# Kernel optimization log

Measured on AMD Instinct MI355X. Metric: run time of the kernel, lower is better.

Reference implementation:

```python
import jax, jax.numpy as jnp
import numpy as np

B, N, T, E, EH, C = 32, 500, 13, 2000, 300, 40
EPS = 1e-5


def _bn_noaffine(x):
    m = x.mean(axis=(0, 2, 3), keepdims=True)
    v = x.var(axis=(0, 2, 3), keepdims=True)
    return (x - m) * jax.lax.rsqrt(v + EPS)


def _bn(x, g, b):
    return g[None, :, None, None] * _bn_noaffine(x) + b[None, :, None, None]


def _conv1x1(x, W, b):
    # x: [B,Cin,N,T], W: [Cout,Cin]
    return jnp.einsum('bcnt,oc->bont', x, W) + b[None, :, None, None]


def _dconv(x, W, b, dil=2):
    # dilated causal conv, kernel (1,2): W [Cout,Cin,2]
    y = jnp.einsum('bcnt,oc->bont', x[..., :-dil], W[:, :, 0])
    y = y + jnp.einsum('bcnt,oc->bont', x[..., dil:], W[:, :, 1])
    return y + b[None, :, None, None]


def setup_inputs() -> dict:
    key = jax.random.key(0)
    ks = jax.random.split(key, 24)
    d = {}
    d['input'] = jax.random.normal(ks[0], (B, 1, N, T), jnp.float32)
    d['A_fwd'] = jax.random.uniform(ks[1], (N, N), jnp.float32) / N
    d['A_bwd'] = jax.random.uniform(ks[2], (N, N), jnp.float32) / N
    d['indices'] = jax.random.randint(ks[3], (2, E), 0, N, jnp.int32)
    d['G0_all'] = jax.random.uniform(ks[4], (E, EH), jnp.float32) * 0.01
    d['G1_all'] = jax.random.uniform(ks[5], (EH, E), jnp.float32) * 0.01
    d['nodevec1'] = jax.random.normal(ks[6], (N, 10), jnp.float32)
    d['nodevec2'] = jax.random.normal(ks[7], (10, N), jnp.float32)
    d['w_edge_f'] = jax.random.uniform(ks[8], (EH,), jnp.float32)
    d['w_edge_b'] = jax.random.uniform(ks[9], (EH,), jnp.float32)
    d['vsrc_f'] = jax.random.normal(ks[10], (3, C), jnp.float32) * 0.05
    d['vdst_f'] = jax.random.normal(ks[11], (3, C), jnp.float32) * 0.05
    d['vsrc_b'] = jax.random.normal(ks[12], (3, C), jnp.float32) * 0.05
    d['vdst_b'] = jax.random.normal(ks[13], (3, C), jnp.float32) * 0.05
    d['start_w'] = jax.random.normal(ks[14], (C, 1), jnp.float32)
    d['start_b'] = jnp.zeros((C,), jnp.float32)
    d['filter_w'] = jax.random.normal(ks[15], (3, C, C, 2), jnp.float32) * (1.0 / np.sqrt(2 * C))
    d['filter_b'] = jnp.zeros((3, C), jnp.float32)
    d['gate_w'] = jax.random.normal(ks[16], (3, C, C, 2), jnp.float32) * (1.0 / np.sqrt(2 * C))
    d['gate_b'] = jnp.zeros((3, C), jnp.float32)
    d['gconv_w'] = jax.random.normal(ks[17], (3, 7 * C, C), jnp.float32) * (1.0 / np.sqrt(7 * C))
    d['gconv_b'] = jnp.zeros((3, C), jnp.float32)
    d['bn_g_gamma'] = jnp.ones((3, C), jnp.float32)
    d['bn_g_beta'] = jnp.zeros((3, C), jnp.float32)
    d['bn_gamma'] = jnp.ones((3, C), jnp.float32)
    d['bn_beta'] = jnp.zeros((3, C), jnp.float32)
    d['skip_w'] = jax.random.normal(ks[18], (3, 320, C), jnp.float32) * (1.0 / np.sqrt(C))
    d['skip_b'] = jnp.zeros((3, 320), jnp.float32)
    d['end1_w'] = jax.random.normal(ks[19], (640, 320), jnp.float32) * (1.0 / np.sqrt(320))
    d['end1_b'] = jnp.zeros((640,), jnp.float32)
    d['end2_w'] = jax.random.normal(ks[20], (12, 640), jnp.float32) * (1.0 / np.sqrt(640))
    d['end2_b'] = jnp.zeros((12,), jnp.float32)
    return d


def reference(input, A_fwd, A_bwd, indices, G0_all, G1_all, nodevec1, nodevec2,
              w_edge_f, w_edge_b, vsrc_f, vdst_f, vsrc_b, vdst_b,
              start_w, start_b, filter_w, filter_b, gate_w, gate_b,
              gconv_w, gconv_b, bn_g_gamma, bn_g_beta, bn_gamma, bn_beta,
              skip_w, skip_b, end1_w, end1_b, end2_w, end2_b):
    x = _bn_noaffine(input)
    x = _conv1x1(x, start_w, start_b)
    b, _, n, _ = x.shape
    # adaptive adjacency: softmax(relu(V1 @ V2)) over rows (torch dim=1 on [N,N])
    adp = jax.nn.softmax(jax.nn.relu(nodevec1 @ nodevec2), axis=1)
    # hypergraph edge-to-edge diffusion operators: G0 @ diag(w) @ G1  ->  [E,E]
    GG_f = G0_all @ (w_edge_f[:, None] * G1_all)
    GG_b = G0_all @ (w_edge_b[:, None] * G1_all)
    i0, i1 = indices[0], indices[1]
    eye = jnp.eye(n, dtype=x.dtype)
    skip = None
    for blk in range(3):
        # dynamic edge scores from node features (mean over time)
        xmean = x.mean(axis=3)                              # [B,C,N]
        src = xmean[:, :, i0]                               # [B,C,E]
        dst = xmean[:, :, i1]
        sc_f = jnp.einsum('bce,c->be', src, vsrc_f[blk]) + jnp.einsum('bce,c->be', dst, vdst_f[blk])
        sc_b = jnp.einsum('bce,c->be', src, vsrc_b[blk]) + jnp.einsum('bce,c->be', dst, vdst_b[blk])
        ef = jax.nn.sigmoid(sc_f @ GG_f)                    # [B,E]
        eb = jax.nn.sigmoid(sc_b @ GG_b)
        # identity medium with sigmoid edge weights scattered at the edge indices
        Mf = jnp.broadcast_to(eye, (b, n, n)).at[:, i0, i1].set(ef)
        Mb = jnp.broadcast_to(eye, (b, n, n)).at[:, i0, i1].set(eb)
        s0 = Mf * A_fwd[None]                               # [B,N,N]
        s1 = jnp.swapaxes(Mb, 1, 2) * A_bwd[None]
        s2 = jnp.broadcast_to(adp, (b, n, n))
        residual = x
        f = jnp.tanh(_dconv(residual, filter_w[blk], filter_b[blk]))
        g = jax.nn.sigmoid(_dconv(residual, gate_w[blk], gate_b[blk]))
        x = f * g
        # diffusion graph conv, order 2, over 3 batched supports
        outs = [x]
        for A in (s0, s1, s2):
            x1 = jnp.einsum('bcnt,bnm->bcmt', x, A)
            outs.append(x1)
            outs.append(jnp.einsum('bcnt,bnm->bcmt', x1, A))
        h = jnp.concatenate(outs, axis=1)                   # [B,7C,N,T']
        x = jnp.einsum('bcnt,co->bont', h, gconv_w[blk]) + gconv_b[blk][None, :, None, None]
        x = _bn(x, bn_g_gamma[blk], bn_g_beta[blk])
        x = x + residual[:, :, :, -x.shape[3]:]
        x = _bn(x, bn_gamma[blk], bn_beta[blk])
        s = _conv1x1(x, skip_w[blk], skip_b[blk])
        skip = s if skip is None else s + skip[:, :, :, -s.shape[3]:]
    x = jax.nn.leaky_relu(skip)
    x = jax.nn.leaky_relu(_conv1x1(x, end1_w, end1_b))
    x = _conv1x1(x, end2_w, end2_b)
    return x
```

## Files before the change

### kernel.cpp

```cpp
#include <hip/hip_runtime.h>
#include <hip/hip_bf16.h>

constexpr int B_  = 32;
constexpr int N_  = 500;
constexpr int T0_ = 13;
constexpr int E_  = 2000;
constexpr int EH_ = 300;
constexpr int C_  = 40;
constexpr float EPS_ = 1e-5f;
constexpr int KP_ = 512;

typedef short bf16x8 __attribute__((ext_vector_type(8)));
typedef _Float16 f16x8 __attribute__((ext_vector_type(8)));
typedef float f32x4  __attribute__((ext_vector_type(4)));

__device__ __forceinline__ float sigm(float x){ return 1.f/(1.f+__expf(-x)); }
__device__ __forceinline__ float lrelu(float x){ return x > 0.f ? x : 0.01f*x; }
__device__ __forceinline__ unsigned short f2bf(float f){
    __hip_bfloat16 h = __float2bfloat16(f);
    return *(unsigned short*)&h;
}
__device__ __forceinline__ float bf2f(unsigned short us){
    __hip_bfloat16 h = *(__hip_bfloat16*)&us;
    return __bfloat162float(h);
}

__global__ __launch_bounds__(256) void kern_init(float* __restrict__ insum, int* __restrict__ map,
                                                 int* __restrict__ cnts, int* __restrict__ selfe,
                                                 int* __restrict__ adpTbz)
{
    int i = blockIdx.x*256 + threadIdx.x;
    if (i < 2) insum[i] = 0.f;
    if (i < N_*N_) map[i] = -1;
    if (i < 1024) cnts[i] = 0;
    if (i < 512) selfe[i] = -1;
    if (i < KP_*KP_/2) adpTbz[i] = 0;
}

__global__ __launch_bounds__(256) void kern_zeroacc(float* __restrict__ p, int n)
{
    int i = blockIdx.x*256 + threadIdx.x;
    if (i < n) p[i] = 0.f;
}

__global__ __launch_bounds__(256) void kern_instats(const float* __restrict__ in, float* __restrict__ acc)
{
    float s = 0.f, ss = 0.f;
    int total = B_*N_*T0_;
    for (int i = blockIdx.x*256 + threadIdx.x; i < total; i += gridDim.x*256) {
        float v = in[i]; s += v; ss += v*v;
    }
    __shared__ float l1[256], l2[256];
    l1[threadIdx.x] = s; l2[threadIdx.x] = ss; __syncthreads();
    for (int o = 128; o > 0; o >>= 1) {
        if (threadIdx.x < o) { l1[threadIdx.x] += l1[threadIdx.x+o]; l2[threadIdx.x] += l2[threadIdx.x+o]; }
        __syncthreads();
    }
    if (threadIdx.x == 0) { atomicAdd(&acc[0], l1[0]); atomicAdd(&acc[1], l2[0]); }
}

__global__ __launch_bounds__(256) void kern_x0(const float* __restrict__ in, const float* __restrict__ insum,
    const float* __restrict__ sw, const float* __restrict__ sb, float* __restrict__ x)
{
    int idx = blockIdx.x*256 + threadIdx.x;
    int total = B_*N_*T0_*C_;
    if (idx >= total) return;
    float cnt = (float)(B_*N_*T0_);
    float mean = insum[0]/cnt;
    float var  = insum[1]/cnt - mean*mean;
    float inv  = rsqrtf(var + EPS_);
    int c = idx % C_;
    int pos = idx / C_;
    float xn = (in[pos] - mean)*inv;
    x[idx] = sw[c]*xn + sb[c];
}

__global__ __launch_bounds__(512) void kern_adp(const float* __restrict__ nv1, const float* __restrict__ nv2,
                                                __hip_bfloat16* __restrict__ adpTb)
{
    int n = blockIdx.x;
    int m = threadIdx.x;
    float r = 0.f;
    if (m < N_) {
        #pragma unroll
        for (int k = 0; k < 10; ++k) r += nv1[n*10+k]*nv2[k*N_+m];
        r = r > 0.f ? r : 0.f;
    }
    __shared__ float red[512];
    red[threadIdx.x] = (m < N_) ? r : -1e30f; __syncthreads();
    for (int o = 256; o > 0; o >>= 1) {
        if (threadIdx.x < o) red[threadIdx.x] = fmaxf(red[threadIdx.x], red[threadIdx.x+o]);
        __syncthreads();
    }
    float mx = red[0]; __syncthreads();
    float ev = (m < N_) ? __expf(r - mx) : 0.f;
    red[threadIdx.x] = ev; __syncthreads();
    for (int o = 256; o > 0; o >>= 1) {
        if (threadIdx.x < o) red[threadIdx.x] += red[threadIdx.x+o];
        __syncthreads();
    }
    float sum = red[0];
    if (m < N_) adpTb[(size_t)m*KP_ + n] = __float2bfloat16(ev/sum);
}

__global__ void kern_emax(const int* __restrict__ idx, int* __restrict__ map)
{
    int e = blockIdx.x*256 + threadIdx.x;
    if (e < E_) atomicMax(&map[idx[e]*N_ + idx[E_+e]], e);
}
__global__ void kern_ecnt(const int* __restrict__ idx, const int* __restrict__ map,
                          int* __restrict__ cnt0, int* __restrict__ cnt1, int* __restrict__ selfe)
{
    int e = blockIdx.x*256 + threadIdx.x;
    if (e >= E_) return;
    int i0 = idx[e], i1 = idx[E_+e];
    if (map[i0*N_+i1] != e) return;
    atomicAdd(&cnt1[i1], 1);
    atomicAdd(&cnt0[i0], 1);
    if (i0 == i1) selfe[i0] = e;
}
__global__ __launch_bounds__(512) void kern_scan(const int* __restrict__ cnt0, const int* __restrict__ cnt1,
    int* __restrict__ ptr0, int* __restrict__ ptr1, int* __restrict__ cur0, int* __restrict__ cur1)
{
    __shared__ int s0[512], s1[512];
    int tid = threadIdx.x;
    s0[tid] = (tid < N_) ? cnt0[tid] : 0;
    s1[tid] = (tid < N_) ? cnt1[tid] : 0;
    __syncthreads();
    for (int o = 1; o < 512; o <<= 1) {
        int v0 = (tid >= o) ? s0[tid-o] : 0;
        int v1 = (tid >= o) ? s1[tid-o] : 0;
        __syncthreads();
        s0[tid] += v0; s1[tid] += v1;
        __syncthreads();
    }
    if (tid == 0) { ptr0[0] = 0; ptr1[0] = 0; }
    if (tid < N_) {
        ptr0[tid+1] = s0[tid]; ptr1[tid+1] = s1[tid];
        cur0[tid] = (tid == 0) ? 0 : s0[tid-1];
        cur1[tid] = (tid == 0) ? 0 : s1[tid-1];
    }
}
__global__ void kern_efill(const int* __restrict__ idx, const int* __restrict__ map,
    const float* __restrict__ Af, const float* __restrict__ Ab,
    int* __restrict__ cur0, int* __restrict__ cur1,
    int* __restrict__ e0id, int* __restrict__ e0nb, float* __restrict__ a0v,
    int* __restrict__ e1id, int* __restrict__ e1nb, float* __restrict__ a1v)
{
    int e = blockIdx.x*256 + threadIdx.x;
    if (e >= E_) return;
    int i0 = idx[e], i1 = idx[E_+e];
    if (map[i0*N_+i1] != e) return;
    int s1 = atomicAdd(&cur1[i1], 1);
    e0id[s1] = e; e0nb[s1] = i0; a0v[s1] = Af[i0*N_+i1];
    int s0 = atomicAdd(&cur0[i0], 1);
    e1id[s0] = e; e1nb[s0] = i1; a1v[s0] = Ab[i1*N_+i0];
}

__global__ __launch_bounds__(64) void kern_umean(const float* __restrict__ x, int Tin,
    const float* __restrict__ vsf, const float* __restrict__ vdf,
    const float* __restrict__ vsb, const float* __restrict__ vdb,
    float* __restrict__ usf, float* __restrict__ udf, float* __restrict__ usb, float* __restrict__ udb)
{
    int bn = blockIdx.x;
    const float* xp = x + (size_t)bn*Tin*C_;
    int tid = threadIdx.x;
    float a0=0.f,a1=0.f,a2=0.f,a3=0.f;
    for (int i = tid; i < Tin*C_; i += 64) {
        float v = xp[i]; int c = i % C_;
        a0 += v*vsf[c]; a1 += v*vdf[c]; a2 += v*vsb[c]; a3 += v*vdb[c];
    }
    for (int o = 32; o > 0; o >>= 1) {
        a0 += __shfl_down(a0,o); a1 += __shfl_down(a1,o);
        a2 += __shfl_down(a2,o); a3 += __shfl_down(a3,o);
    }
    if (tid == 0) {
        float inv = 1.f/(float)Tin;
        usf[bn]=a0*inv; udf[bn]=a1*inv; usb[bn]=a2*inv; udb[bn]=a3*inv;
    }
}

__global__ void kern_sc(const int* __restrict__ idx,
    const float* __restrict__ usf, const float* __restrict__ udf,
    const float* __restrict__ usb, const float* __restrict__ udb,
    float* __restrict__ scf, float* __restrict__ scb)
{
    int i = blockIdx.x*256 + threadIdx.x;
    if (i >= B_*E_) return;
    int b = i / E_, e = i % E_;
    int i0 = idx[e], i1 = idx[E_+e];
    scf[i] = usf[b*N_+i0] + udf[b*N_+i1];
    scb[i] = usb[b*N_+i0] + udb[b*N_+i1];
}

__global__ __launch_bounds__(320) void kern_t(const float* __restrict__ scf, const float* __restrict__ scb,
    const float* __restrict__ G0, float* __restrict__ tf, float* __restrict__ tb)
{
    int b = blockIdx.x, chunk = blockIdx.y;
    int e0 = chunk*250;
    __shared__ float sf[250], sb2[250];
    int tid = threadIdx.x;
    for (int i = tid; i < 250; i += 320) { sf[i] = scf[b*E_+e0+i]; sb2[i] = scb[b*E_+e0+i]; }
    __syncthreads();
    if (tid < EH_) {
        float af = 0.f, ab = 0.f;
        for (int i = 0; i < 250; ++i) {
            float g = G0[(size_t)(e0+i)*EH_ + tid];
            af += sf[i]*g; ab += sb2[i]*g;
        }
        atomicAdd(&tf[b*EH_+tid], af);
        atomicAdd(&tb[b*EH_+tid], ab);
    }
}

__global__ __launch_bounds__(256) void kern_ef(const float* __restrict__ tf, const float* __restrict__ tb,
    const float* __restrict__ wf, const float* __restrict__ wb, const float* __restrict__ G1,
    float* __restrict__ ef, float* __restrict__ eb)
{
    int b = blockIdx.y;
    int e = blockIdx.x*256 + threadIdx.x;
    __shared__ float f[EH_], g[EH_];
    for (int i = threadIdx.x; i < EH_; i += 256) {
        f[i] = tf[b*EH_+i]*wf[i];
        g[i] = tb[b*EH_+i]*wb[i];
    }
    __syncthreads();
    if (e < E_) {
        float af = 0.f, ab = 0.f;
        for (int h = 0; h < EH_; ++h) {
            float v = G1[(size_t)h*E_ + e];
            af += f[h]*v; ab += g[h]*v;
        }
        ef[b*E_+e] = sigm(af);
        eb[b*E_+e] = sigm(ab);
    }
}

__global__ __launch_bounds__(256) void kern_dconv_acc(const float* __restrict__ x, int Tin,
    const float* __restrict__ fw, const float* __restrict__ fb4,
    const float* __restrict__ gw, const float* __restrict__ gb4,
    const float* __restrict__ wl0, const float* __restrict__ gbias,
    float* __restrict__ xg, float* __restrict__ gc,
    __hip_bfloat16* __restrict__ xgT, int JP)
{
    int Tout = Tin - 2;
    int nout = Tout*C_;
    int tile = threadIdx.x >> 7;
    int lane = threadIdx.x & 127;
    int bn = blockIdx.x*2 + tile;
    int b = bn / N_, n = bn % N_;
    __shared__ alignas(16) float xs[2][T0_*C_];
    __shared__ alignas(16) float wf[2*C_*C_];
    __shared__ alignas(16) float wg[2*C_*C_];
    __shared__ alignas(16) float wl[C_*C_];
    __shared__ alignas(16) float ps[2][11*C_];
    int tid = threadIdx.x;
    {
        const float4* xp = (const float4*)(x + (size_t)bn*Tin*C_);
        float4* xd = (float4*)xs[tile];
        for (int i = lane; i < (Tin*C_)/4; i += 128) xd[i] = xp[i];
    }
    for (int i = tid; i < 2*C_*C_; i += 256) {
        int k = i / (C_*C_); int r = i % (C_*C_); int c = r / C_; int o = r % C_;
        wf[i] = fw[(o*C_+c)*2 + k];
        wg[i] = gw[(o*C_+c)*2 + k];
    }
    for (int i = tid; i < C_*C_; i += 256) wl[i] = wl0[i];
    __syncthreads();
    int nq = Tout*10;
    for (int u = lane; u < nq; u += 128) {
        int t = u/10, o = (u%10)*4;
        float4 f4 = *(const float4*)&fb4[o];
        float4 g4 = *(const float4*)&gb4[o];
        for (int c = 0; c < C_; ++c) {
            float x0v = xs[tile][t*C_+c], x2v = xs[tile][(t+2)*C_+c];
            float4 wf0 = *(const float4*)&wf[c*C_+o];
            float4 wf1 = *(const float4*)&wf[C_*C_ + c*C_+o];
            float4 wg0 = *(const float4*)&wg[c*C_+o];
            float4 wg1 = *(const float4*)&wg[C_*C_ + c*C_+o];
            f4.x += wf0.x*x0v + wf1.x*x2v;  f4.y += wf0.y*x0v + wf1.y*x2v;
            f4.z += wf0.z*x0v + wf1.z*x2v;  f4.w += wf0.w*x0v + wf1.w*x2v;
            g4.x += wg0.x*x0v + wg1.x*x2v;  g4.y += wg0.y*x0v + wg1.y*x2v;
            g4.z += wg0.z*x0v + wg1.z*x2v;  g4.w += wg0.w*x0v + wg1.w*x2v;
        }
        float4 r4;
        r4.x = tanhf(f4.x)*sigm(g4.x);
        r4.y = tanhf(f4.y)*sigm(g4.y);
        r4.z = tanhf(f4.z)*sigm(g4.z);
        r4.w = tanhf(f4.w)*sigm(g4.w);
        *(float4*)&ps[tile][t*C_+o] = r4;
        *(float4*)&xg[(size_t)bn*nout + t*C_+o] = r4;
        int j = t*C_+o;
        size_t tb = ((size_t)b*JP + j)*KP_ + n;
        xgT[tb]          = __float2bfloat16(r4.x);
        xgT[tb + KP_]    = __float2bfloat16(r4.y);
        xgT[tb + 2*KP_]  = __float2bfloat16(r4.z);
        xgT[tb + 3*KP_]  = __float2bfloat16(r4.w);
    }
    __syncthreads();
    for (int u = lane; u < nq; u += 128) {
        int t = u/10, o = (u%10)*4;
        float4 a4 = *(const float4*)&gbias[o];
        for (int c = 0; c < C_; ++c) {
            float s = ps[tile][t*C_+c];
            float4 w = *(const float4*)&wl[c*C_+o];
            a4.x += s*w.x; a4.y += s*w.y; a4.z += s*w.z; a4.w += s*w.w;
        }
        *(float4*)&gc[(size_t)bn*nout + t*C_+o] = a4;
    }
}

__global__ __launch_bounds__(256) void kern_sparse_acc(const float* __restrict__ in,
    float* __restrict__ outTile, int Tout,
    const int* __restrict__ ptr, const int* __restrict__ nbr, const int* __restrict__ eid,
    const float* __restrict__ aval, const float* __restrict__ coef,
    const float* __restrict__ Amat, const int* __restrict__ selfe,
    const float* __restrict__ gwp, float* __restrict__ gc)
{
    int tile = threadIdx.x >> 7;
    int lane = threadIdx.x & 127;
    int bn = blockIdx.x*2 + tile;
    int b = bn / N_, m = bn % N_;
    __shared__ float wv[2][64];
    __shared__ int   nb[2][64];
    __shared__ alignas(16) float ps[2][11*C_];
    __shared__ alignas(16) float wl[C_*C_];
    int tid = threadIdx.x;
    int p0 = ptr[m], p1 = ptr[m+1];
    int deg = p1 - p0; if (deg > 64) deg = 64;
    if (lane < deg) {
        wv[tile][lane] = coef[b*E_ + eid[p0+lane]] * aval[p0+lane];
        nb[tile][lane] = nbr[p0+lane];
    }
    for (int i = tid; i < C_*C_; i += 256) wl[i] = gwp[i];
    __syncthreads();
    float dval = (selfe[m] >= 0) ? 0.f : Amat[(size_t)m*N_ + m];
    const float* inb = in + (size_t)b*N_*Tout*C_;
    int nout = Tout*C_;
    for (int oi = lane; oi < nout; oi += 128) {
        float acc = dval * inb[(size_t)m*nout + oi];
        for (int j = 0; j < deg; ++j) acc += wv[tile][j]*inb[(size_t)nb[tile][j]*nout + oi];
        ps[tile][oi] = acc;
        if (outTile) outTile[(size_t)bn*nout + oi] = acc;
    }
    __syncthreads();
    int nq = Tout*10;
    for (int u = lane; u < nq; u += 128) {
        int t = u/10, o = (u%10)*4;
        float4 a4 = *(const float4*)&gc[(size_t)bn*nout + t*C_+o];
        for (int c = 0; c < C_; ++c) {
            float s = ps[tile][t*C_+c];
            float4 w = *(const float4*)&wl[c*C_+o];
            a4.x += s*w.x; a4.y += s*w.y; a4.z += s*w.z; a4.w += s*w.w;
        }
        *(float4*)&gc[(size_t)bn*nout + t*C_+o] = a4;
    }
}

__global__ __launch_bounds__(256) void kern_gemm_mfma(const __hip_bfloat16* __restrict__ adpTb,
    const __hip_bfloat16* __restrict__ inT, float* __restrict__ outF,
    __hip_bfloat16* __restrict__ outT, int LD, int JP)
{
    int tid = threadIdx.x;
    int wave = tid >> 6, lane = tid & 63;
    int rn = lane & 15, q = lane >> 4;
    int b = blockIdx.z;
    int m0 = blockIdx.x*64;
    int j0 = blockIdx.y*64;
    const short* Ap = (const short*)adpTb + (size_t)(m0 + wave*16 + rn)*KP_ + q*8;
    bf16x8 areg[16];
    #pragma unroll
    for (int kk = 0; kk < 16; ++kk) areg[kk] = *(const bf16x8*)(Ap + kk*32);
    const short* Bp = (const short*)inT + ((size_t)b*JP + j0 + rn)*KP_ + q*8;
    f32x4 acc[4] = {};
    #pragma unroll
    for (int kk = 0; kk < 16; ++kk) {
        #pragma unroll
        for (int s = 0; s < 4; ++s) {
            bf16x8 bb = *(const bf16x8*)(Bp + (size_t)s*16*KP_ + kk*32);
            acc[s] = __builtin_amdgcn_mfma_f32_16x16x32_bf16(areg[kk], bb, acc[s], 0, 0, 0);
        }
    }
    int mb = m0 + wave*16 + q*4;
    #pragma unroll
    for (int s = 0; s < 4; ++s) {
        int j = j0 + s*16 + rn;
        if (j >= LD) continue;
        #pragma unroll
        for (int r = 0; r < 4; ++r) {
            int m = mb + r;
            if (m < N_) outF[((size_t)b*N_ + m)*LD + j] = acc[s][r];
        }
        if (outT) {
            ushort4 v;
            v.x = f2bf(acc[s][0]); v.y = f2bf(acc[s][1]);
            v.z = f2bf(acc[s][2]); v.w = f2bf(acc[s][3]);
            *(ushort4*)((unsigned short*)outT + ((size_t)b*JP + j)*KP_ + mb) = v;
        }
    }
}

__global__ __launch_bounds__(256) void kern_gacc(const float* __restrict__ part, const float* __restrict__ gwp,
    float* __restrict__ gc, int Tout)
{
    int tile = threadIdx.x >> 7;
    int lane = threadIdx.x & 127;
    int bn = blockIdx.x*2 + tile;
    int nout = Tout*C_;
    __shared__ alignas(16) float ps[2][11*C_];
    __shared__ alignas(16) float wl[C_*C_];
    int tid = threadIdx.x;
    {
        const float4* pp = (const float4*)(part + (size_t)bn*nout);
        float4* pd = (float4*)ps[tile];
        for (int i = lane; i < nout/4; i += 128) pd[i] = pp[i];
    }
    for (int i = tid; i < C_*C_; i += 256) wl[i] = gwp[i];
    __syncthreads();
    int nq = Tout*10;
    for (int u = lane; u < nq; u += 128) {
        int t = u/10, o = (u%10)*4;
        float4 a4 = *(const float4*)&gc[(size_t)bn*nout + t*C_+o];
        for (int c = 0; c < C_; ++c) {
            float s = ps[tile][t*C_+c];
            float4 w = *(const float4*)&wl[c*C_+o];
            a4.x += s*w.x; a4.y += s*w.y; a4.z += s*w.z; a4.w += s*w.w;
        }
        *(float4*)&gc[(size_t)bn*nout + t*C_+o] = a4;
    }
}

__global__ __launch_bounds__(320) void kern_bnstats(const float* __restrict__ src, size_t total, float* __restrict__ acc)
{
    int tid = threadIdx.x;
    float s = 0.f, ss = 0.f;
    for (size_t i = (size_t)blockIdx.x*320 + tid; i < total; i += (size_t)gridDim.x*320) {
        float v = src[i]; s += v; ss += v*v;
    }
    __shared__ float ls[320], lss[320];
    ls[tid] = s; lss[tid] = ss; __syncthreads();
    if (tid < C_) {
        float t1 = 0.f, t2 = 0.f;
        for (int r = 0; r < 8; ++r) { t1 += ls[r*C_+tid]; t2 += lss[r*C_+tid]; }
        atomicAdd(&acc[tid], t1); atomicAdd(&acc[C_+tid], t2);
    }
}

__global__ __launch_bounds__(320) void kern_bn1(float* __restrict__ gc, const float* __restrict__ resid,
    int Tin, int Tout, const float* __restrict__ acc1,
    const float* __restrict__ g1, const float* __restrict__ b1, float* __restrict__ acc2)
{
    int tid = threadIdx.x; int c = tid % C_;
    float cnt = (float)(B_*N_*Tout);
    float mean = acc1[c]/cnt;
    float var  = acc1[C_+c]/cnt - mean*mean;
    float inv  = rsqrtf(var + EPS_);
    float gg = g1[c], bb = b1[c];
    int dlt = Tin - Tout;
    float s = 0.f, ss = 0.f;
    size_t total = (size_t)B_*N_*Tout*C_;
    for (size_t i = (size_t)blockIdx.x*320 + tid; i < total; i += (size_t)gridDim.x*320) {
        size_t pos = i / C_; int t = (int)(pos % Tout); size_t bn = pos / Tout;
        float y = gg*(gc[i]-mean)*inv + bb;
        y += resid[(bn*Tin + (t+dlt))*C_ + c];
        gc[i] = y;
        s += y; ss += y*y;
    }
    __shared__ float ls[320], lss[320];
    ls[tid] = s; lss[tid] = ss; __syncthreads();
    if (tid < C_) {
        float t1 = 0.f, t2 = 0.f;
        for (int r = 0; r < 8; ++r) { t1 += ls[r*C_+tid]; t2 += lss[r*C_+tid]; }
        atomicAdd(&acc2[tid], t1); atomicAdd(&acc2[C_+tid], t2);
    }
}

__global__ __launch_bounds__(256) void kern_bn2(const float* __restrict__ gc, float* __restrict__ xout, int Tout,
    const float* __restrict__ acc2, const float* __restrict__ g2, const float* __restrict__ b2)
{
    size_t total = (size_t)B_*N_*Tout*C_;
    size_t i = (size_t)blockIdx.x*256 + threadIdx.x;
    if (i >= total) return;
    int c = (int)(i % C_);
    float cnt = (float)(B_*N_*Tout);
    float mean = acc2[c]/cnt;
    float var  = acc2[C_+c]/cnt - mean*mean;
    float inv  = rsqrtf(var + EPS_);
    xout[i] = g2[c]*(gc[i]-mean)*inv + b2[c];
}

__global__ __launch_bounds__(256) void kern_skip(const float* __restrict__ x, int Tout,
    const float* __restrict__ sw, const float* __restrict__ sbias, __hip_bfloat16* __restrict__ skp, int first)
{
    int bn0 = blockIdx.x*4; int half = blockIdx.y;
    int off = Tout - 7;
    __shared__ alignas(16) float xs[4][7*C_];
    __shared__ alignas(16) float wl[C_*164];
    int tid = threadIdx.x;
    for (int i = tid; i < 4*(7*C_/4); i += 256) {
        int bl = i / 70, r = i % 70;
        ((float4*)xs[bl])[r] = ((const float4*)(x + ((size_t)(bn0+bl)*Tout + off)*C_))[r];
    }
    for (int i = tid; i < 160*C_; i += 256) {
        int oo = i / C_, c = i % C_;
        wl[c*164 + oo] = sw[(size_t)(half*160 + oo)*C_ + c];
    }
    __syncthreads();
    for (int u = tid; u < 4*7*40; u += 256) {
        int bl = u / 280; int v = u % 280;
        int t = v / 40, o = (v % 40)*4;
        float4 a4 = {0.f,0.f,0.f,0.f};
        for (int c = 0; c < C_; ++c) {
            float s = xs[bl][t*C_+c];
            float4 w = *(const float4*)&wl[c*164 + o];
            a4.x += s*w.x; a4.y += s*w.y; a4.z += s*w.z; a4.w += s*w.w;
        }
        int og = half*160 + o;
        float4 b4 = *(const float4*)&sbias[og];
        a4.x += b4.x; a4.y += b4.y; a4.z += b4.z; a4.w += b4.w;
        size_t di = ((size_t)(bn0+bl)*7 + t)*320 + og;
        if (first) {
            skp[di+0] = __float2bfloat16(a4.x);
            skp[di+1] = __float2bfloat16(a4.y);
            skp[di+2] = __float2bfloat16(a4.z);
            skp[di+3] = __float2bfloat16(a4.w);
        } else {
            skp[di+0] = __float2bfloat16(__bfloat162float(skp[di+0]) + a4.x);
            skp[di+1] = __float2bfloat16(__bfloat162float(skp[di+1]) + a4.y);
            skp[di+2] = __float2bfloat16(__bfloat162float(skp[di+2]) + a4.z);
            skp[di+3] = __float2bfloat16(__bfloat162float(skp[di+3]) + a4.w);
        }
    }
}

__global__ __launch_bounds__(256) void kern_cvtw(const float* __restrict__ w, __hip_bfloat16* __restrict__ wb, int n)
{
    int i = blockIdx.x*256 + threadIdx.x;
    if (i < n) wb[i] = __float2bfloat16(w[i]);
}

constexpr int ASD_ = 324;
__global__ __launch_bounds__(256) void kern_end2(const __hip_bfloat16* __restrict__ skp,
    const __hip_bfloat16* __restrict__ e1wb, const float* __restrict__ e1b,
    const float* __restrict__ e2w, const float* __restrict__ e2b, float* __restrict__ out)
{
    __shared__ short As[64*ASD_];
    __shared__ _Float16 w2h[640][12];
    int tid = threadIdx.x;
    int wave = tid >> 6, lane = tid & 63;
    int rn = lane & 15, q = lane >> 4;
    int m0 = blockIdx.x*64;
    {
        const bf16x8* gA = (const bf16x8*)((const short*)skp + (size_t)m0*320);
        for (int i = tid; i < 2560; i += 256) {
            bf16x8 v = gA[i];
            int row = i / 40, col = (i % 40)*8;
            *(bf16x8*)&As[row*ASD_ + col] = v;
        }
    }
    for (int i = tid; i < 640*12; i += 256) {
        int c = i / 12, o = i % 12;
        w2h[c][o] = (_Float16)e2w[o*640 + c];
    }
    __syncthreads();
    bf16x8 areg[10];
    {
        const short* Arow = As + (wave*16 + rn)*ASD_ + q*8;
        #pragma unroll
        for (int kk = 0; kk < 10; ++kk) {
            bf16x8 v = *(const bf16x8*)(Arow + kk*32);
            bf16x8 r;
            #pragma unroll
            for (int e = 0; e < 8; ++e)
                r[e] = (short)f2bf(lrelu(bf2f((unsigned short)v[e])));
            areg[kk] = r;
        }
    }
    float acc_out[4][12] = {};
    const short* e1p = (const short*)e1wb;
    for (int csp = 0; csp < 20; ++csp) {
        const short* Bp0 = e1p + (size_t)(csp*32 + rn)*320 + q*8;
        const short* Bp1 = Bp0 + 16*320;
        f32x4 c00 = {}, c01 = {}, c10 = {}, c11 = {};
        #pragma unroll
        for (int kk = 0; kk < 10; kk += 2) {
            bf16x8 b00 = *(const bf16x8*)(Bp0 + kk*32);
            bf16x8 b01 = *(const bf16x8*)(Bp0 + (kk+1)*32);
            bf16x8 b10 = *(const bf16x8*)(Bp1 + kk*32);
            bf16x8 b11 = *(const bf16x8*)(Bp1 + (kk+1)*32);
            c00 = __builtin_amdgcn_mfma_f32_16x16x32_bf16(areg[kk],   b00, c00, 0, 0, 0);
            c10 = __builtin_amdgcn_mfma_f32_16x16x32_bf16(areg[kk],   b10, c10, 0, 0, 0);
            c01 = __builtin_amdgcn_mfma_f32_16x16x32_bf16(areg[kk+1], b01, c01, 0, 0, 0);
            c11 = __builtin_amdgcn_mfma_f32_16x16x32_bf16(areg[kk+1], b11, c11, 0, 0, 0);
        }
        int ca = csp*32 + rn, cb = ca + 16;
        float bias0 = e1b[ca], bias1 = e1b[cb];
        float wa[12], wb[12];
        #pragma unroll
        for (int o = 0; o < 12; ++o) { wa[o] = (float)w2h[ca][o]; wb[o] = (float)w2h[cb][o]; }
        #pragma unroll
        for (int r = 0; r < 4; ++r) {
            float y0 = lrelu(c00[r] + c01[r] + bias0);
            float y1 = lrelu(c10[r] + c11[r] + bias1);
            #pragma unroll
            for (int o = 0; o < 12; ++o)
                acc_out[r][o] += y0*wa[o] + y1*wb[o];
        }
    }
    #pragma unroll
    for (int r = 0; r < 4; ++r)
        #pragma unroll
        for (int o = 0; o < 12; ++o) {
            float v = acc_out[r][o];
            v += __shfl_xor(v, 1);
            v += __shfl_xor(v, 2);
            v += __shfl_xor(v, 4);
            v += __shfl_xor(v, 8);
            acc_out[r][o] = v;
        }
    if (rn < 12) {
        float bo = e2b[rn];
        #pragma unroll
        for (int r = 0; r < 4; ++r) {
            int gm = m0 + wave*16 + q*4 + r;
            int t = gm % 7; int bn = gm / 7; int n = bn % N_; int b = bn / N_;
            out[(((size_t)b*12 + rn)*N_ + n)*7 + t] = acc_out[r][rn] + bo;
        }
    }
}

extern "C" void kernel_launch(void* const* d_in, const int* in_sizes, int n_in,
                              void* d_out, int out_size, void* d_ws, size_t ws_size,
                              hipStream_t stream)
{
    (void)in_sizes; (void)n_in; (void)out_size;
    const float* input   = (const float*)d_in[0];
    const float* A_fwd   = (const float*)d_in[1];
    const float* A_bwd   = (const float*)d_in[2];
    const int*   indices = (const int*)  d_in[3];
    const float* G0      = (const float*)d_in[4];
    const float* G1      = (const float*)d_in[5];
    const float* nv1     = (const float*)d_in[6];
    const float* nv2     = (const float*)d_in[7];
    const float* wef     = (const float*)d_in[8];
    const float* web     = (const float*)d_in[9];
    const float* vsf     = (const float*)d_in[10];
    const float* vdf     = (const float*)d_in[11];
    const float* vsb     = (const float*)d_in[12];
    const float* vdb     = (const float*)d_in[13];
    const float* start_w = (const float*)d_in[14];
    const float* start_b = (const float*)d_in[15];
    const float* filt_w  = (const float*)d_in[16];
    const float* filt_b  = (const float*)d_in[17];
    const float* gate_w  = (const float*)d_in[18];
    const float* gate_b  = (const float*)d_in[19];
    const float* gcw     = (const float*)d_in[20];
    const float* gcb     = (const float*)d_in[21];
    const float* bng_g   = (const float*)d_in[22];
    const float* bng_b   = (const float*)d_in[23];
    const float* bn_g    = (const float*)d_in[24];
    const float* bn_b    = (const float*)d_in[25];
    const float* skw     = (const float*)d_in[26];
    const float* skb     = (const float*)d_in[27];
    const float* e1w     = (const float*)d_in[28];
    const float* e1b     = (const float*)d_in[29];
    const float* e2w     = (const float*)d_in[30];
    const float* e2b     = (const float*)d_in[31];
    float* out = (float*)d_out;

    float* W = (float*)d_ws;
    size_t off = 0;
    auto FA = [&](size_t n){ off = (off + 3) & ~(size_t)3; float* p = W + off; off += n; return p; };
    float* insum  = FA(2);
    float* tf     = FA((size_t)B_*EH_);
    float* tb     = FA((size_t)B_*EH_);
    float* bnacc1 = FA(80);
    float* bnacc2 = FA(80);
    float* usf = FA((size_t)B_*N_); float* udf = FA((size_t)B_*N_);
    float* usb = FA((size_t)B_*N_); float* udb = FA((size_t)B_*N_);
    float* scf = FA((size_t)B_*E_); float* scb = FA((size_t)B_*E_);
    float* efv = FA((size_t)B_*E_); float* ebv = FA((size_t)B_*E_);
    __hip_bfloat16* adpTb = (__hip_bfloat16*)FA((size_t)KP_*KP_/2);
    float* a0v = FA(E_); float* a1v = FA(E_);
    int* map  = (int*)FA((size_t)N_*N_);
    int* cnt0 = (int*)FA(512); int* cnt1 = (int*)FA(512);
    int* ptr0 = (int*)FA(512); int* ptr1 = (int*)FA(512);
    int* cur0 = (int*)FA(512); int* cur1 = (int*)FA(512);
    int* selfe = (int*)FA(512);
    int* e0id = (int*)FA(E_); int* e0nb = (int*)FA(E_);
    int* e1id = (int*)FA(E_); int* e1nb = (int*)FA(E_);
    float* xA  = FA((size_t)B_*N_*T0_*C_);
    float* xg  = FA((size_t)B_*N_*11*C_);
    float* pa  = FA((size_t)B_*N_*11*C_);
    float* gc  = FA((size_t)B_*N_*11*C_);
    __hip_bfloat16* skp = (__hip_bfloat16*)FA((size_t)B_*N_*7*320/2);
    __hip_bfloat16* xgT = (__hip_bfloat16*)FA((size_t)B_*448*KP_/2);
    __hip_bfloat16* paT = (__hip_bfloat16*)FA((size_t)B_*448*KP_/2);
    __hip_bfloat16* e1wb = (__hip_bfloat16*)xg;

    if (ws_size < off*sizeof(float)) return;

    kern_init<<<(N_*N_+255)/256, 256, 0, stream>>>(insum, map, cnt0, selfe, (int*)adpTb);
    kern_instats<<<256, 256, 0, stream>>>(input, insum);
    kern_x0<<<(B_*N_*T0_*C_+255)/256, 256, 0, stream>>>(input, insum, start_w, start_b, xA);
    kern_adp<<<N_, 512, 0, stream>>>(nv1, nv2, adpTb);
    kern_emax<<<(E_+255)/256, 256, 0, stream>>>(indices, map);
    kern_ecnt<<<(E_+255)/256, 256, 0, stream>>>(indices, map, cnt0, cnt1, selfe);
    kern_scan<<<1, 512, 0, stream>>>(cnt0, cnt1, ptr0, ptr1, cur0, cur1);
    kern_efill<<<(E_+255)/256, 256, 0, stream>>>(indices, map, A_fwd, A_bwd, cur0, cur1,
                                                 e0id, e0nb, a0v, e1id, e1nb, a1v);

    for (int blk = 0; blk < 3; ++blk) {
        int Tin = T0_ - 2*blk;
        int Tout = Tin - 2;
        int LD = Tout*C_;
        int JP = (LD + 63) & ~63;
        size_t total = (size_t)B_*N_*Tout*C_;
        kern_zeroacc<<<(2*B_*EH_+160+255)/256, 256, 0, stream>>>(tf, 2*B_*EH_+160);

        kern_umean<<<B_*N_, 64, 0, stream>>>(xA, Tin, vsf+blk*C_, vdf+blk*C_, vsb+blk*C_, vdb+blk*C_,
                                             usf, udf, usb, udb);
        kern_sc<<<(B_*E_+255)/256, 256, 0, stream>>>(indices, usf, udf, usb, udb, scf, scb);
        kern_t<<<dim3(B_, 8), 320, 0, stream>>>(scf, scb, G0, tf, tb);
        kern_ef<<<dim3(8, B_), 256, 0, stream>>>(tf, tb, wef, web, G1, efv, ebv);

        const float* gwb = gcw + (size_t)blk*7*C_*C_;
        kern_dconv_acc<<<B_*N_/2, 256, 0, stream>>>(xA, Tin,
            filt_w + (size_t)blk*2*C_*C_, filt_b + blk*C_,
            gate_w + (size_t)blk*2*C_*C_, gate_b + blk*C_,
            gwb + 0*C_*C_, gcb + blk*C_, xg, gc, xgT, JP);
        kern_sparse_acc<<<B_*N_/2, 256, 0, stream>>>(xg, pa, Tout, ptr1, e0nb, e0id, a0v, efv,
                                                     A_fwd, selfe, gwb + 1*C_*C_, gc);
        kern_sparse_acc<<<B_*N_/2, 256, 0, stream>>>(pa, nullptr, Tout, ptr1, e0nb, e0id, a0v, efv,
                                                     A_fwd, selfe, gwb + 2*C_*C_, gc);
        kern_sparse_acc<<<B_*N_/2, 256, 0, stream>>>(xg, pa, Tout, ptr0, e1nb, e1id, a1v, ebv,
                                                     A_bwd, selfe, gwb + 3*C_*C_, gc);
        kern_sparse_acc<<<B_*N_/2, 256, 0, stream>>>(pa, nullptr, Tout, ptr0, e1nb, e1id, a1v, ebv,
                                                     A_bwd, selfe, gwb + 4*C_*C_, gc);
        dim3 gg(8, JP/64, B_);
        kern_gemm_mfma<<<gg, 256, 0, stream>>>(adpTb, xgT, pa, paT, LD, JP);
        kern_gacc<<<B_*N_/2, 256, 0, stream>>>(pa, gwb + 5*C_*C_, gc, Tout);
        kern_gemm_mfma<<<gg, 256, 0, stream>>>(adpTb, paT, xg, nullptr, LD, JP);
        kern_gacc<<<B_*N_/2, 256, 0, stream>>>(xg, gwb + 6*C_*C_, gc, Tout);

        kern_bnstats<<<512, 320, 0, stream>>>(gc, total, bnacc1);
        kern_bn1<<<512, 320, 0, stream>>>(gc, xA, Tin, Tout, bnacc1, bng_g + blk*C_, bng_b + blk*C_, bnacc2);
        kern_bn2<<<(int)((total+255)/256), 256, 0, stream>>>(gc, xA, Tout, bnacc2, bn_g + blk*C_, bn_b + blk*C_);

        kern_skip<<<dim3(B_*N_/4, 2), 256, 0, stream>>>(xA, Tout, skw + (size_t)blk*320*C_, skb + blk*320,
                                                        skp, blk == 0 ? 1 : 0);
    }

    kern_cvtw<<<(640*320+255)/256, 256, 0, stream>>>(e1w, e1wb, 640*320);
    kern_end2<<<B_*N_*7/64, 256, 0, stream>>>(skp, e1wb, e1b, e2w, e2b, out);
}
```

Measured before the change: 2.604 ms.

## Fuse edge-score into kern_t, fold last BN into skip, tune end2

The edge-score computation moves into kern_t, which removes one launch per block while still writing scf/scb. In the last block, the second batch-norm is folded into kern_skip as a per-channel scale and bias applied on load, so kern_bn2 and its full-tensor write are skipped. kern_end2 now applies leaky-relu once during the shared-memory fill instead of per wave, gets launch_bounds with min 2 blocks, and loads its f16 weight rows as vectors with the csp loop kept rolled. The launch bound may raise register pressure or cause spills.

```diff
diff --git a/kernel.cpp b/kernel.cpp
--- a/kernel.cpp
+++ b/kernel.cpp
@@ -12,6 +12,7 @@
 
 typedef short bf16x8 __attribute__((ext_vector_type(8)));
 typedef _Float16 f16x8 __attribute__((ext_vector_type(8)));
+typedef _Float16 f16x4 __attribute__((ext_vector_type(4)));
 typedef float f32x4  __attribute__((ext_vector_type(4)));
 
 __device__ __forceinline__ float sigm(float x){ return 1.f/(1.f+__expf(-x)); }
@@ -180,27 +181,24 @@
     }
 }
 
-__global__ void kern_sc(const int* __restrict__ idx,
+__global__ __launch_bounds__(320) void kern_t(const int* __restrict__ idx,
     const float* __restrict__ usf, const float* __restrict__ udf,
     const float* __restrict__ usb, const float* __restrict__ udb,
+    const float* __restrict__ G0, float* __restrict__ tf, float* __restrict__ tb,
     float* __restrict__ scf, float* __restrict__ scb)
-{
-    int i = blockIdx.x*256 + threadIdx.x;
-    if (i >= B_*E_) return;
-    int b = i / E_, e = i % E_;
-    int i0 = idx[e], i1 = idx[E_+e];
-    scf[i] = usf[b*N_+i0] + udf[b*N_+i1];
-    scb[i] = usb[b*N_+i0] + udb[b*N_+i1];
-}
-
-__global__ __launch_bounds__(320) void kern_t(const float* __restrict__ scf, const float* __restrict__ scb,
-    const float* __restrict__ G0, float* __restrict__ tf, float* __restrict__ tb)
 {
     int b = blockIdx.x, chunk = blockIdx.y;
     int e0 = chunk*250;
     __shared__ float sf[250], sb2[250];
     int tid = threadIdx.x;
-    for (int i = tid; i < 250; i += 320) { sf[i] = scf[b*E_+e0+i]; sb2[i] = scb[b*E_+e0+i]; }
+    for (int i = tid; i < 250; i += 320) {
+        int e = e0 + i;
+        int i0 = idx[e], i1 = idx[E_+e];
+        float vf = usf[b*N_+i0] + udf[b*N_+i1];
+        float vb = usb[b*N_+i0] + udb[b*N_+i1];
+        sf[i] = vf; sb2[i] = vb;
+        scf[b*E_+e] = vf; scb[b*E_+e] = vb;
+    }
     __syncthreads();
     if (tid < EH_) {
         float af = 0.f, ab = 0.f;
@@ -490,16 +488,37 @@
 }
 
 __global__ __launch_bounds__(256) void kern_skip(const float* __restrict__ x, int Tout,
-    const float* __restrict__ sw, const float* __restrict__ sbias, __hip_bfloat16* __restrict__ skp, int first)
+    const float* __restrict__ sw, const float* __restrict__ sbias, __hip_bfloat16* __restrict__ skp, int first,
+    const float* __restrict__ acc2, const float* __restrict__ g2, const float* __restrict__ b2)
 {
     int bn0 = blockIdx.x*4; int half = blockIdx.y;
     int off = Tout - 7;
     __shared__ alignas(16) float xs[4][7*C_];
     __shared__ alignas(16) float wl[C_*164];
-    int tid = threadIdx.x;
+    __shared__ float scl[C_], bia[C_];
+    int tid = threadIdx.x;
+    if (acc2) {
+        if (tid < C_) {
+            float cnt = (float)(B_*N_*Tout);
+            float mean = acc2[tid]/cnt;
+            float var  = acc2[C_+tid]/cnt - mean*mean;
+            float inv  = rsqrtf(var + EPS_);
+            scl[tid] = g2[tid]*inv;
+            bia[tid] = b2[tid] - g2[tid]*mean*inv;
+        }
+        __syncthreads();
+    }
     for (int i = tid; i < 4*(7*C_/4); i += 256) {
         int bl = i / 70, r = i % 70;
-        ((float4*)xs[bl])[r] = ((const float4*)(x + ((size_t)(bn0+bl)*Tout + off)*C_))[r];
+        float4 v = ((const float4*)(x + ((size_t)(bn0+bl)*Tout + off)*C_))[r];
+        if (acc2) {
+            int c0 = (r*4) % C_;
+            v.x = scl[c0]*v.x + bia[c0];
+            v.y = scl[c0+1]*v.y + bia[c0+1];
+            v.z = scl[c0+2]*v.z + bia[c0+2];
+            v.w = scl[c0+3]*v.w + bia[c0+3];
+        }
+        ((float4*)xs[bl])[r] = v;
     }
     for (int i = tid; i < 160*C_; i += 256) {
         int oo = i / C_, c = i % C_;
@@ -540,7 +559,7 @@
 }
 
 constexpr int ASD_ = 324;
-__global__ __launch_bounds__(256) void kern_end2(const __hip_bfloat16* __restrict__ skp,
+__global__ __launch_bounds__(256, 2) void kern_end2(const __hip_bfloat16* __restrict__ skp,
     const __hip_bfloat16* __restrict__ e1wb, const float* __restrict__ e1b,
     const float* __restrict__ e2w, const float* __restrict__ e2b, float* __restrict__ out)
 {
@@ -554,30 +573,28 @@
         const bf16x8* gA = (const bf16x8*)((const short*)skp + (size_t)m0*320);
         for (int i = tid; i < 2560; i += 256) {
             bf16x8 v = gA[i];
-            int row = i / 40, col = (i % 40)*8;
-            *(bf16x8*)&As[row*ASD_ + col] = v;
-        }
-    }
-    for (int i = tid; i < 640*12; i += 256) {
-        int c = i / 12, o = i % 12;
-        w2h[c][o] = (_Float16)e2w[o*640 + c];
-    }
-    __syncthreads();
-    bf16x8 areg[10];
-    {
-        const short* Arow = As + (wave*16 + rn)*ASD_ + q*8;
-        #pragma unroll
-        for (int kk = 0; kk < 10; ++kk) {
-            bf16x8 v = *(const bf16x8*)(Arow + kk*32);
             bf16x8 r;
             #pragma unroll
             for (int e = 0; e < 8; ++e)
                 r[e] = (short)f2bf(lrelu(bf2f((unsigned short)v[e])));
-            areg[kk] = r;
-        }
+            int row = i / 40, col = (i % 40)*8;
+            *(bf16x8*)&As[row*ASD_ + col] = r;
+        }
+    }
+    for (int i = tid; i < 640*12; i += 256) {
+        int c = i / 12, o = i % 12;
+        w2h[c][o] = (_Float16)e2w[o*640 + c];
+    }
+    __syncthreads();
+    bf16x8 areg[10];
+    {
+        const short* Arow = As + (wave*16 + rn)*ASD_ + q*8;
+        #pragma unroll
+        for (int kk = 0; kk < 10; ++kk) areg[kk] = *(const bf16x8*)(Arow + kk*32);
     }
     float acc_out[4][12] = {};
     const short* e1p = (const short*)e1wb;
+    #pragma unroll 1
     for (int csp = 0; csp < 20; ++csp) {
         const short* Bp0 = e1p + (size_t)(csp*32 + rn)*320 + q*8;
         const short* Bp1 = Bp0 + 16*320;
@@ -595,9 +612,18 @@
         }
         int ca = csp*32 + rn, cb = ca + 16;
         float bias0 = e1b[ca], bias1 = e1b[cb];
+        f16x4 wa0 = *(const f16x4*)&w2h[ca][0];
+        f16x4 wa1 = *(const f16x4*)&w2h[ca][4];
+        f16x4 wa2 = *(const f16x4*)&w2h[ca][8];
+        f16x4 wb0 = *(const f16x4*)&w2h[cb][0];
+        f16x4 wb1 = *(const f16x4*)&w2h[cb][4];
+        f16x4 wb2 = *(const f16x4*)&w2h[cb][8];
         float wa[12], wb[12];
         #pragma unroll
-        for (int o = 0; o < 12; ++o) { wa[o] = (float)w2h[ca][o]; wb[o] = (float)w2h[cb][o]; }
+        for (int o = 0; o < 4; ++o) {
+            wa[o] = (float)wa0[o]; wa[4+o] = (float)wa1[o]; wa[8+o] = (float)wa2[o];
+            wb[o] = (float)wb0[o]; wb[4+o] = (float)wb1[o]; wb[8+o] = (float)wb2[o];
+        }
         #pragma unroll
         for (int r = 0; r < 4; ++r) {
             float y0 = lrelu(c00[r] + c01[r] + bias0);
@@ -720,8 +746,7 @@
 
         kern_umean<<<B_*N_, 64, 0, stream>>>(xA, Tin, vsf+blk*C_, vdf+blk*C_, vsb+blk*C_, vdb+blk*C_,
                                              usf, udf, usb, udb);
-        kern_sc<<<(B_*E_+255)/256, 256, 0, stream>>>(indices, usf, udf, usb, udb, scf, scb);
-        kern_t<<<dim3(B_, 8), 320, 0, stream>>>(scf, scb, G0, tf, tb);
+        kern_t<<<dim3(B_, 8), 320, 0, stream>>>(indices, usf, udf, usb, udb, G0, tf, tb, scf, scb);
         kern_ef<<<dim3(8, B_), 256, 0, stream>>>(tf, tb, wef, web, G1, efv, ebv);
 
         const float* gwb = gcw + (size_t)blk*7*C_*C_;
@@ -745,10 +770,14 @@
 
         kern_bnstats<<<512, 320, 0, stream>>>(gc, total, bnacc1);
         kern_bn1<<<512, 320, 0, stream>>>(gc, xA, Tin, Tout, bnacc1, bng_g + blk*C_, bng_b + blk*C_, bnacc2);
-        kern_bn2<<<(int)((total+255)/256), 256, 0, stream>>>(gc, xA, Tout, bnacc2, bn_g + blk*C_, bn_b + blk*C_);
-
-        kern_skip<<<dim3(B_*N_/4, 2), 256, 0, stream>>>(xA, Tout, skw + (size_t)blk*320*C_, skb + blk*320,
-                                                        skp, blk == 0 ? 1 : 0);
+        if (blk < 2) {
+            kern_bn2<<<(int)((total+255)/256), 256, 0, stream>>>(gc, xA, Tout, bnacc2, bn_g + blk*C_, bn_b + blk*C_);
+            kern_skip<<<dim3(B_*N_/4, 2), 256, 0, stream>>>(xA, Tout, skw + (size_t)blk*320*C_, skb + blk*320,
+                                                            skp, blk == 0 ? 1 : 0, nullptr, nullptr, nullptr);
+        } else {
+            kern_skip<<<dim3(B_*N_/4, 2), 256, 0, stream>>>(gc, Tout, skw + (size_t)blk*320*C_, skb + blk*320,
+                                                            skp, 0, bnacc2, bn_g + blk*C_, bn_b + blk*C_);
+        }
     }
 
     kern_cvtw<<<(640*320+255)/256, 256, 0, stream>>>(e1w, e1wb, 640*320);
```

Result: faster. 2.523 ms (-3.1%).
